# Kernel optimization log

Measured on AMD Instinct MI355X. Metric: run time of the kernel, lower is better.

Reference implementation:

```python
import math
import jax, jax.numpy as jnp
from jax import lax
import numpy as np

C, H, W, N, K = 256, 64, 64, 16, 7

def setup_inputs() -> dict:
    key = jax.random.key(0)
    k0, k1, k2, k3, k4 = jax.random.split(key, 5)
    x = jax.random.normal(k0, (N, C, H, W), dtype=jnp.float32)
    p_2_w = 0.02 * jax.random.normal(k1, (1, C, H, 1), dtype=jnp.float32)
    # nn.Conv2d(c, c, (1,5), groups=1, bias=False) -> weight [c, c, 1, 5]
    fan_in = C * 1 * 5
    bound = 1.0 / math.sqrt(fan_in)
    p_3_w = jax.random.uniform(k2, (C, C, 1, 5), dtype=jnp.float32, minval=-bound, maxval=bound)
    p_4_w = 0.02 * jax.random.normal(k3, (1, C, K, 1, 1), dtype=jnp.float32)
    p_6_w = jax.random.uniform(k4, (K, 1), dtype=jnp.float32, minval=-7.0, maxval=7.0)
    return {"x": x, "p_2_w": p_2_w, "p_3_w": p_3_w, "p_4_w": p_4_w, "p_6_w": p_6_w}

def reference(x, p_2_w, p_3_w, p_4_w, p_6_w):
    n, c, h, w = x.shape
    k = p_4_w.shape[2]  # 7 taps
    pad = (k - 1) // 2
    # F.unfold with kernel (1,7), pad (0,3): stack 7 width-shifted copies -> [n,c,7,h,w]
    xp = jnp.pad(x, ((0, 0), (0, 0), (0, 0), (pad, pad)))
    t_1 = jnp.stack([xp[..., i:i + w] for i in range(k)], axis=2)
    # per-(channel,row) scaling then dense 1x5 conv
    t_2 = p_2_w * x
    t_3 = lax.conv_general_dilated(
        t_2, p_3_w, window_strides=(1, 1), padding=[(0, 0), (2, 2)],
        dimension_numbers=("NCHW", "OIHW", "NCHW"))
    # weighted tap-sum: (p_4_w * t_1) contracted over taps with p_6_w[:,0]
    t_4 = p_4_w * t_1
    t_6 = jnp.einsum("nckhw,kf->ncfhw", t_4, p_6_w)[:, :, 0]  # [n,c,h,w]
    t_5 = jax.nn.relu(x)
    s = h * w
    # channel-attention matrix [n,c,c]
    t_7 = jnp.einsum("ncs,nds->ncd", t_3.reshape(n, c, s), t_6.reshape(n, c, s))
    t_7 = t_7 * (1.0 / math.sqrt(s))
    # bmm(t_5^T, t_7) -> [n,s,d]; permuting to [n,d,h,w] == einsum 'ncs,ncd->nds'
    out = jnp.einsum("ncs,ncd->nds", t_5.reshape(n, c, s), t_7)
    out = out * (1.0 / math.sqrt(c))
    return out.reshape(n, c, h, w)
```

## Files before the change

kernel.cpp:

```cpp
#include <hip/hip_runtime.h>
#include <hip/hip_bf16.h>

typedef __attribute__((ext_vector_type(8))) short bf16x8;
typedef __attribute__((ext_vector_type(4))) float f32x4;

#define NB 16
#define CD 256
#define HD 64
#define WD 64
#define WP 68
#define SD 4096
#define KU 1280

__device__ __forceinline__ void gload16(const void* g, void* lds) {
  __builtin_amdgcn_global_load_lds(
      (const __attribute__((address_space(1))) unsigned int*)g,
      (__attribute__((address_space(3))) unsigned int*)lds, 16, 0, 0);
}

__global__ __launch_bounds__(256) void prep_w3(const float* __restrict__ p3,
                                               __hip_bfloat16* __restrict__ A) {
  int id = blockIdx.x * 256 + threadIdx.x;
  if (id >= CD * KU) return;
  int o = id / KU;
  int r = id - o * KU;
  int j = r >> 8;
  int c = r & 255;
  A[id] = __float2bfloat16(p3[(o * CD + c) * 5 + j]);
}

__global__ __launch_bounds__(256) void prep_x(const float* __restrict__ x,
                                              const float* __restrict__ p2,
                                              const float* __restrict__ p4,
                                              const float* __restrict__ p6,
                                              __hip_bfloat16* __restrict__ t2p,
                                              __hip_bfloat16* __restrict__ t5T,
                                              __hip_bfloat16* __restrict__ t6) {
  int h = blockIdx.x;
  int c0 = blockIdx.y * 64;
  int n = blockIdx.z;
  __shared__ float xl[64][67];
  __shared__ float p2l[64];
  __shared__ float wtl[64][8];
  int t = threadIdx.x;

  if (t < 64) p2l[t] = p2[(c0 + t) * HD + h];
  for (int idx = t; idx < 448; idx += 256) {
    int c = idx / 7, k = idx - c * 7;
    wtl[c][k] = p4[(c0 + c) * 7 + k] * p6[k];
  }

  {
    int cq = t >> 4;
    int w4 = (t & 15) * 4;
#pragma unroll
    for (int cc = 0; cc < 4; ++cc) {
      int cl = cc * 16 + cq;
      const float4 xv = *reinterpret_cast<const float4*>(
          &x[(((size_t)n * CD + c0 + cl) * HD + h) * WD + w4]);
      xl[cl][w4 + 0] = xv.x;
      xl[cl][w4 + 1] = xv.y;
      xl[cl][w4 + 2] = xv.z;
      xl[cl][w4 + 3] = xv.w;
    }
  }
  __syncthreads();

  __hip_bfloat16* t2pn = t2p + (size_t)n * HD * WP * CD;
#pragma unroll
  for (int ii = 0; ii < 2; ++ii) {
    int w = (t >> 3) + ii * 32;
    int cb = (t & 7) * 8;
    __hip_bfloat16 o2[8], o5[8];
#pragma unroll
    for (int j = 0; j < 8; ++j) {
      float xv = xl[cb + j][w];
      o5[j] = __float2bfloat16(fmaxf(xv, 0.f));
      o2[j] = __float2bfloat16(p2l[cb + j] * xv);
    }
    size_t s = (size_t)h * 64 + w;
    *reinterpret_cast<bf16x8*>(&t5T[((size_t)n * SD + s) * CD + c0 + cb]) =
        *reinterpret_cast<const bf16x8*>(o5);
    *reinterpret_cast<bf16x8*>(&t2pn[((size_t)h * WP + w + 2) * CD + c0 + cb]) =
        *reinterpret_cast<const bf16x8*>(o2);
  }
  if (t < 32) {
    int pi = t >> 3;
    int wp = (pi < 2) ? pi : pi + 64;
    int cb = (t & 7) * 8;
    bf16x8 z = (bf16x8){0, 0, 0, 0, 0, 0, 0, 0};
    *reinterpret_cast<bf16x8*>(&t2pn[((size_t)h * WP + wp) * CD + c0 + cb]) = z;
  }

#pragma unroll
  for (int ii = 0; ii < 2; ++ii) {
    int cl = (t >> 3) + ii * 32;
    int w8 = (t & 7) * 8;
    float hx[14];
#pragma unroll
    for (int m = 0; m < 14; ++m) {
      int wi = w8 - 3 + m;
      hx[m] = (wi >= 0 && wi < 64) ? xl[cl][wi] : 0.f;
    }
    float wt[7];
#pragma unroll
    for (int k = 0; k < 7; ++k) wt[k] = wtl[cl][k];
    __hip_bfloat16 o6[8];
#pragma unroll
    for (int u = 0; u < 8; ++u) {
      float acc = 0.f;
#pragma unroll
      for (int k = 0; k < 7; ++k) acc += wt[k] * hx[u + k];
      o6[u] = __float2bfloat16(acc);
    }
    *reinterpret_cast<bf16x8*>(&t6[((size_t)n * CD + c0 + cl) * SD + h * 64 + w8]) =
        *reinterpret_cast<const bf16x8*>(o6);
  }
}

#define STAGE_A(c, kt, d)                                                              \
  gload16(Ab + (size_t)((c) * 64 + wv * 8 + (lane >> 3)) * 2560 + (kt) * 128 + cbsrc,  \
          (char*)lds + (d) * 65536 + (c) * 8192 + wv * 1024)
#define STAGE_B(j, kt, d)                                                              \
  gload16(t2pb + (size_t)(s0 + (j) * 64 + wv * 8 + (lane >> 3) + 4 * (sb * 4 + (j))) * 512 + \
                     (kt) * 128 + cbsrc,                                               \
          (char*)lds + (d) * 65536 + 32768 + (j) * 8192 + wv * 1024)

#define LDAV(d, MH, AV)                                                                \
  do {                                                                                 \
    const __hip_bfloat16* pA =                                                         \
        lds + (d) * 32768 + (wm * 128 + (MH) * 64 + l16) * 64;                         \
    _Pragma("unroll") for (int ks = 0; ks < 2; ++ks) {                                 \
      int cb = (ks * 32 + lg * 8) ^ lxor;                                              \
      _Pragma("unroll") for (int mf = 0; mf < 4; ++mf)                                 \
          AV[ks * 4 + mf] = *reinterpret_cast<const bf16x8*>(pA + mf * 1024 + cb);     \
    }                                                                                  \
  } while (0)

#define LDBV(d, NH, BV)                                                                \
  do {                                                                                 \
    const __hip_bfloat16* pB =                                                         \
        lds + (d) * 32768 + 16384 + (wn * 64 + (NH) * 32 + l16) * 64;                  \
    _Pragma("unroll") for (int ks = 0; ks < 2; ++ks) {                                 \
      int cb = (ks * 32 + lg * 8) ^ lxor;                                              \
      _Pragma("unroll") for (int nf = 0; nf < 2; ++nf)                                 \
          BV[ks * 2 + nf] = *reinterpret_cast<const bf16x8*>(pB + nf * 1024 + cb);     \
    }                                                                                  \
  } while (0)

#define MFMAQ(MH, NH, AV, BV)                                                          \
  do {                                                                                 \
    __builtin_amdgcn_s_setprio(1);                                                     \
    _Pragma("unroll") for (int ks = 0; ks < 2; ++ks)                                   \
        _Pragma("unroll") for (int mf = 0; mf < 4; ++mf)                               \
            _Pragma("unroll") for (int nf = 0; nf < 2; ++nf)                           \
                acc[(MH) * 4 + mf][(NH) * 2 + nf] = __builtin_amdgcn_mfma_f32_16x16x32_bf16( \
                    AV[ks * 4 + mf], BV[ks * 2 + nf], acc[(MH) * 4 + mf][(NH) * 2 + nf], \
                    0, 0, 0);                                                          \
    __builtin_amdgcn_s_setprio(0);                                                     \
  } while (0)

#define VMWAIT(N) asm volatile("s_waitcnt vmcnt(" #N ")" ::: "memory")
#define BARRIER() __builtin_amdgcn_s_barrier()

__global__ __launch_bounds__(512, 2) void gemm_b8(const __hip_bfloat16* __restrict__ A,
                                                  const __hip_bfloat16* __restrict__ t2p,
                                                  __hip_bfloat16* __restrict__ t3) {
  __shared__ __align__(16) __hip_bfloat16 lds[65536];
  const int n = blockIdx.z;
  const int sb = blockIdx.x;
  const int t = threadIdx.x;
  const int wv = t >> 6, lane = t & 63;
  const int wm = wv >> 2, wn = wv & 3;
  const int l16 = lane & 15, lg = lane >> 4;
  const int s0 = sb * 256;
  const char* Ab = (const char*)A;
  const char* t2pb = (const char*)(t2p + (size_t)n * HD * WP * CD);
  const int cbsrc = ((lane & 7) ^ (lane >> 3)) * 16;
  const int lxor = (l16 & 7) * 8;

  f32x4 acc[8][4];
#pragma unroll
  for (int i = 0; i < 8; ++i)
#pragma unroll
    for (int j = 0; j < 4; ++j) acc[i][j] = (f32x4){0.f, 0.f, 0.f, 0.f};

  bf16x8 av0[8], av1[8], bvA[4], bvB[4];

  STAGE_B(0, 0, 0); STAGE_B(1, 0, 0); STAGE_B(2, 0, 0); STAGE_B(3, 0, 0);
  STAGE_A(0, 0, 0); STAGE_A(1, 0, 0); STAGE_A(2, 0, 0); STAGE_A(3, 0, 0);
  VMWAIT(0);
  BARRIER();
  LDAV(0, 0, av0);
  LDBV(0, 0, bvA);

  for (int kt = 0; kt < 19; ++kt) {
    const int cur = kt & 1, nxt = cur ^ 1, kn = kt + 1;
    LDAV(cur, 1, av1);
    LDBV(cur, 1, bvB);
    MFMAQ(0, 0, av0, bvA);
    STAGE_B(0, kn, nxt); STAGE_B(1, kn, nxt); STAGE_B(2, kn, nxt); STAGE_B(3, kn, nxt);
    BARRIER();
    MFMAQ(0, 1, av0, bvB);
    STAGE_A(0, kn, nxt); STAGE_A(1, kn, nxt); STAGE_A(2, kn, nxt); STAGE_A(3, kn, nxt);
    BARRIER();
    MFMAQ(1, 0, av1, bvA);
    BARRIER();
    MFMAQ(1, 1, av1, bvB);
    VMWAIT(0);
    BARRIER();
    LDAV(nxt, 0, av0);
    LDBV(nxt, 0, bvA);
  }
  LDAV(1, 1, av1);
  LDBV(1, 1, bvB);
  MFMAQ(0, 0, av0, bvA);
  MFMAQ(0, 1, av0, bvB);
  MFMAQ(1, 0, av1, bvA);
  MFMAQ(1, 1, av1, bvB);

  __hip_bfloat16* t3n = t3 + (size_t)n * CD * SD;
#pragma unroll
  for (int im = 0; im < 8; ++im)
#pragma unroll
    for (int in = 0; in < 4; ++in) {
      int row0 = wm * 128 + im * 16 + lg * 4;
      int col = s0 + wn * 64 + in * 16 + l16;
#pragma unroll
      for (int r = 0; r < 4; ++r)
        t3n[(size_t)(row0 + r) * SD + col] = __float2bfloat16(acc[im][in][r]);
    }
}

__global__ __launch_bounds__(256) void gemm_c_part(const __hip_bfloat16* __restrict__ t6,
                                                   const __hip_bfloat16* __restrict__ t3,
                                                   float* __restrict__ P4) {
  __shared__ __align__(16) __hip_bfloat16 lA[64 * 64];
  __shared__ __align__(16) __hip_bfloat16 lB[64 * 64];
  int bx = blockIdx.x;
  int cbk = bx & 3, kc = bx >> 2;
  int db = blockIdx.y;
  int n = blockIdx.z;
  int t = threadIdx.x;
  int wave = t >> 6, lane = t & 63;
  int wm = wave >> 1, wn = wave & 1;
  int l16 = lane & 15, lg = lane >> 4;
  int d0 = db * 64;
  int c0 = cbk * 64;
  int kbase = kc * 1024;
  const __hip_bfloat16* An = t6 + (size_t)n * CD * SD + kbase;
  const __hip_bfloat16* Bn = t3 + (size_t)n * CD * SD + kbase;

  int srow = t >> 3;
  int scol = (t & 7) * 8;
  const __hip_bfloat16* gA0 = An + (size_t)(d0 + srow) * SD + scol;
  const __hip_bfloat16* gA1 = An + (size_t)(d0 + srow + 32) * SD + scol;
  const __hip_bfloat16* gB0 = Bn + (size_t)(c0 + srow) * SD + scol;
  const __hip_bfloat16* gB1 = Bn + (size_t)(c0 + srow + 32) * SD + scol;
  __hip_bfloat16* lAd0 = &lA[t * 8];
  __hip_bfloat16* lAd1 = &lA[t * 8 + 32 * 64];
  __hip_bfloat16* lBd0 = &lB[t * 8];
  __hip_bfloat16* lBd1 = &lB[t * 8 + 32 * 64];

  f32x4 acc[2][2];
#pragma unroll
  for (int mi = 0; mi < 2; ++mi)
#pragma unroll
    for (int ni = 0; ni < 2; ++ni) acc[mi][ni] = (f32x4){0.f, 0.f, 0.f, 0.f};

  gload16(gA0, lAd0);
  gload16(gA1, lAd1);
  gload16(gB0, lBd0);
  gload16(gB1, lBd1);

  for (int k = 0; k < 16; ++k) {
    __syncthreads();
#pragma unroll
    for (int ks = 0; ks < 2; ++ks) {
      bf16x8 a[2], b[2];
#pragma unroll
      for (int mi = 0; mi < 2; ++mi)
        a[mi] = *reinterpret_cast<const bf16x8*>(&lA[(wm * 32 + mi * 16 + l16) * 64 + ks * 32 + lg * 8]);
#pragma unroll
      for (int ni = 0; ni < 2; ++ni)
        b[ni] = *reinterpret_cast<const bf16x8*>(&lB[(wn * 32 + ni * 16 + l16) * 64 + ks * 32 + lg * 8]);
#pragma unroll
      for (int mi = 0; mi < 2; ++mi)
#pragma unroll
        for (int ni = 0; ni < 2; ++ni)
          acc[mi][ni] = __builtin_amdgcn_mfma_f32_16x16x32_bf16(a[mi], b[ni], acc[mi][ni], 0, 0, 0);
    }
    __syncthreads();
    if (k < 15) {
      int kk = (k + 1) * 64;
      gload16(gA0 + kk, lAd0);
      gload16(gA1 + kk, lAd1);
      gload16(gB0 + kk, lBd0);
      gload16(gB1 + kk, lBd1);
    }
  }

  float* Pn = P4 + ((size_t)kc * NB + n) * CD * CD;
#pragma unroll
  for (int mi = 0; mi < 2; ++mi)
#pragma unroll
    for (int ni = 0; ni < 2; ++ni) {
      int col = c0 + wn * 32 + ni * 16 + l16;
      int row0 = d0 + wm * 32 + mi * 16 + lg * 4;
#pragma unroll
      for (int r = 0; r < 4; ++r)
        Pn[(size_t)(row0 + r) * CD + col] = acc[mi][ni][r];
    }
}

__global__ __launch_bounds__(256) void reduce_P(const float* __restrict__ P4,
                                                __hip_bfloat16* __restrict__ P) {
  size_t i = ((size_t)blockIdx.x * 256 + threadIdx.x) * 4;
  const size_t stride = (size_t)NB * CD * CD;
  float4 a = *reinterpret_cast<const float4*>(P4 + i);
  float4 b = *reinterpret_cast<const float4*>(P4 + stride + i);
  float4 c = *reinterpret_cast<const float4*>(P4 + 2 * stride + i);
  float4 d = *reinterpret_cast<const float4*>(P4 + 3 * stride + i);
  __hip_bfloat16 o[4];
  o[0] = __float2bfloat16((a.x + b.x + c.x + d.x) * 0.015625f);
  o[1] = __float2bfloat16((a.y + b.y + c.y + d.y) * 0.015625f);
  o[2] = __float2bfloat16((a.z + b.z + c.z + d.z) * 0.015625f);
  o[3] = __float2bfloat16((a.w + b.w + c.w + d.w) * 0.015625f);
  *reinterpret_cast<short4*>(&P[i]) = *reinterpret_cast<const short4*>(o);
}

#define DSTAGE_A(i, kk)                                                                \
  gload16(Pb + (size_t)((i) * 32 + wv4 * 8 + (lane >> 3)) * 512 + (kk) * 128 + cbsrc,  \
          (char*)lA + (i) * 4096 + wv4 * 1024)
#define DSTAGE_B(i, kk)                                                                \
  gload16(Tb + (size_t)(s0 + (i) * 32 + wv4 * 8 + (lane >> 3)) * 512 + (kk) * 128 + cbsrc, \
          (char*)lB + (i) * 4096 + wv4 * 1024)

__global__ __launch_bounds__(256, 2) void gemm_d(const __hip_bfloat16* __restrict__ P,
                                                 const __hip_bfloat16* __restrict__ t5T,
                                                 float* __restrict__ out) {
  __shared__ __align__(16) __hip_bfloat16 lA[256 * 64];
  __shared__ __align__(16) __hip_bfloat16 lB[128 * 64];
  const int n = blockIdx.z;
  const int sb = blockIdx.x;
  const int t = threadIdx.x;
  const int wv4 = t >> 6, lane = t & 63;
  const int wm = wv4 >> 1, wn = wv4 & 1;
  const int l16 = lane & 15, lg = lane >> 4;
  const int s0 = sb * 128;
  const char* Pb = (const char*)(P + (size_t)n * CD * CD);
  const char* Tb = (const char*)(t5T + (size_t)n * SD * CD);
  const int cbsrc = ((lane & 7) ^ (lane >> 3)) * 16;
  const int lxor = (l16 & 7) * 8;

  f32x4 acc[8][4];
#pragma unroll
  for (int i = 0; i < 8; ++i)
#pragma unroll
    for (int j = 0; j < 4; ++j) acc[i][j] = (f32x4){0.f, 0.f, 0.f, 0.f};

#pragma unroll
  for (int i = 0; i < 8; ++i) DSTAGE_A(i, 0);
#pragma unroll
  for (int i = 0; i < 4; ++i) DSTAGE_B(i, 0);

  for (int k = 0; k < 4; ++k) {
    __syncthreads();
#pragma unroll
    for (int ks = 0; ks < 2; ++ks) {
      int cb = (ks * 32 + lg * 8) ^ lxor;
      bf16x8 a[8], b[4];
#pragma unroll
      for (int mf = 0; mf < 8; ++mf)
        a[mf] = *reinterpret_cast<const bf16x8*>(&lA[(wm * 128 + mf * 16 + l16) * 64 + cb]);
#pragma unroll
      for (int nf = 0; nf < 4; ++nf)
        b[nf] = *reinterpret_cast<const bf16x8*>(&lB[(wn * 64 + nf * 16 + l16) * 64 + cb]);
#pragma unroll
      for (int mf = 0; mf < 8; ++mf)
#pragma unroll
        for (int nf = 0; nf < 4; ++nf)
          acc[mf][nf] = __builtin_amdgcn_mfma_f32_16x16x32_bf16(a[mf], b[nf], acc[mf][nf], 0, 0, 0);
    }
    __syncthreads();
    if (k < 3) {
      int kk = k + 1;
#pragma unroll
      for (int i = 0; i < 8; ++i) DSTAGE_A(i, kk);
#pragma unroll
      for (int i = 0; i < 4; ++i) DSTAGE_B(i, kk);
    }
  }

  float* outn = out + (size_t)n * CD * SD;
#pragma unroll
  for (int mf = 0; mf < 8; ++mf)
#pragma unroll
    for (int nf = 0; nf < 4; ++nf) {
      int col = s0 + wn * 64 + nf * 16 + l16;
      int row0 = wm * 128 + mf * 16 + lg * 4;
#pragma unroll
      for (int r = 0; r < 4; ++r)
        outn[(size_t)(row0 + r) * SD + col] = acc[mf][nf][r] * 0.0625f;
    }
}

extern "C" void kernel_launch(void* const* d_in, const int* in_sizes, int n_in,
                              void* d_out, int out_size, void* d_ws, size_t ws_size,
                              hipStream_t stream) {
  const float* x = (const float*)d_in[0];
  const float* p2 = (const float*)d_in[1];
  const float* p3 = (const float*)d_in[2];
  const float* p4 = (const float*)d_in[3];
  const float* p6 = (const float*)d_in[4];

  char* ws = (char*)d_ws;
  size_t off = 0;
  __hip_bfloat16* A = (__hip_bfloat16*)(ws + off);
  off += (size_t)CD * KU * 2;
  size_t t2p_off = off;
  __hip_bfloat16* t2p = (__hip_bfloat16*)(ws + off);
  off += (size_t)NB * HD * WP * CD * 2;
  __hip_bfloat16* t5T = (__hip_bfloat16*)(ws + off);
  off += (size_t)NB * SD * CD * 2;
  __hip_bfloat16* t6 = (__hip_bfloat16*)(ws + off);
  off += (size_t)NB * CD * SD * 2;
  __hip_bfloat16* t3 = (__hip_bfloat16*)(ws + off);
  off += (size_t)NB * CD * SD * 2;
  float* P4 = (float*)(ws + t2p_off);
  __hip_bfloat16* P = (__hip_bfloat16*)(ws + t2p_off + (size_t)4 * NB * CD * CD * 4);

  float* out = (float*)d_out;

  prep_w3<<<dim3((CD * KU + 255) / 256), 256, 0, stream>>>(p3, A);
  prep_x<<<dim3(HD, 4, NB), 256, 0, stream>>>(x, p2, p4, p6, t2p, t5T, t6);
  gemm_b8<<<dim3(16, 1, NB), 512, 0, stream>>>(A, t2p, t3);
  gemm_c_part<<<dim3(16, 4, NB), 256, 0, stream>>>(t6, t3, P4);
  reduce_P<<<dim3((NB * CD * CD / 4) / 256), 256, 0, stream>>>(P4, P);
  gemm_d<<<dim3(32, 1, NB), 256, 0, stream>>>(P, t5T, out);
}
```

Baseline: 133.3 us.

## Fold weight prep into prep_x and restructure conv GEMM into 4-stage K=32 pipeline

The separate prep_w3 launch is removed and the bf16 weight conversion is done by the first blocks of prep_x, saving one kernel launch. The main conv GEMM is rewritten from a double-buffered K=64 schedule with multiple barriers per step into a 4-deep ring of K=32 stages with one barrier per stage, a new XOR swizzle, and loads issued two stages ahead. This aims to overlap global-to-LDS traffic with MFMA work and cut barrier count, at the cost of more loop iterations and a different bank-conflict pattern.

```diff
diff --git a/kernel.cpp b/kernel.cpp
--- a/kernel.cpp
+++ b/kernel.cpp
@@ -18,24 +18,15 @@
       (__attribute__((address_space(3))) unsigned int*)lds, 16, 0, 0);
 }
 
-__global__ __launch_bounds__(256) void prep_w3(const float* __restrict__ p3,
-                                               __hip_bfloat16* __restrict__ A) {
-  int id = blockIdx.x * 256 + threadIdx.x;
-  if (id >= CD * KU) return;
-  int o = id / KU;
-  int r = id - o * KU;
-  int j = r >> 8;
-  int c = r & 255;
-  A[id] = __float2bfloat16(p3[(o * CD + c) * 5 + j]);
-}
-
 __global__ __launch_bounds__(256) void prep_x(const float* __restrict__ x,
                                               const float* __restrict__ p2,
                                               const float* __restrict__ p4,
                                               const float* __restrict__ p6,
+                                              const float* __restrict__ p3,
                                               __hip_bfloat16* __restrict__ t2p,
                                               __hip_bfloat16* __restrict__ t5T,
-                                              __hip_bfloat16* __restrict__ t6) {
+                                              __hip_bfloat16* __restrict__ t6,
+                                              __hip_bfloat16* __restrict__ A) {
   int h = blockIdx.x;
   int c0 = blockIdx.y * 64;
   int n = blockIdx.z;
@@ -43,6 +34,18 @@
   __shared__ float p2l[64];
   __shared__ float wtl[64][8];
   int t = threadIdx.x;
+
+  {
+    int bid = (n * 64 + h) * 4 + blockIdx.y;
+    int id = bid * 256 + t;
+    if (id < CD * KU) {
+      int o = id / KU;
+      int r = id - o * KU;
+      int j = r >> 8;
+      int c = r & 255;
+      A[id] = __float2bfloat16(p3[(o * CD + c) * 5 + j]);
+    }
+  }
 
   if (t < 64) p2l[t] = p2[(c0 + t) * HD + h];
   for (int idx = t; idx < 448; idx += 256) {
@@ -118,55 +121,47 @@
   }
 }
 
-#define STAGE_A(c, kt, d)                                                              \
-  gload16(Ab + (size_t)((c) * 64 + wv * 8 + (lane >> 3)) * 2560 + (kt) * 128 + cbsrc,  \
-          (char*)lds + (d) * 65536 + (c) * 8192 + wv * 1024)
-#define STAGE_B(j, kt, d)                                                              \
-  gload16(t2pb + (size_t)(s0 + (j) * 64 + wv * 8 + (lane >> 3) + 4 * (sb * 4 + (j))) * 512 + \
-                     (kt) * 128 + cbsrc,                                               \
-          (char*)lds + (d) * 65536 + 32768 + (j) * 8192 + wv * 1024)
-
-#define LDAV(d, MH, AV)                                                                \
+#define VMWAIT(N) asm volatile("s_waitcnt vmcnt(" #N ")" ::: "memory")
+#define BARRIER() __builtin_amdgcn_s_barrier()
+
+#define ST4(kt, bi)                                                                    \
   do {                                                                                 \
-    const __hip_bfloat16* pA =                                                         \
-        lds + (d) * 32768 + (wm * 128 + (MH) * 64 + l16) * 64;                         \
-    _Pragma("unroll") for (int ks = 0; ks < 2; ++ks) {                                 \
-      int cb = (ks * 32 + lg * 8) ^ lxor;                                              \
-      _Pragma("unroll") for (int mf = 0; mf < 4; ++mf)                                 \
-          AV[ks * 4 + mf] = *reinterpret_cast<const bf16x8*>(pA + mf * 1024 + cb);     \
+    char* dst = lb + ((bi) << 15) + t * 16;                                            \
+    gload16(gA0 + (kt) * 64, dst);                                                     \
+    gload16(gA1 + (kt) * 64, dst + 8192);                                              \
+    gload16(gB0 + (kt) * 64, dst + 16384);                                             \
+    gload16(gB1 + (kt) * 64, dst + 24576);                                             \
+  } while (0)
+
+#define LDF(bi, AV, BV)                                                                \
+  do {                                                                                 \
+    const char* ba = lb + ((bi) << 15);                                                \
+    _Pragma("unroll") for (int mf = 0; mf < 8; ++mf) {                                 \
+      int row = wm * 128 + mf * 16 + l16;                                              \
+      AV[mf] = *reinterpret_cast<const bf16x8*>(ba + row * 64 + ((lg ^ rxor) * 16));   \
+    }                                                                                  \
+    _Pragma("unroll") for (int nf = 0; nf < 4; ++nf) {                                 \
+      int row = wn * 64 + nf * 16 + l16;                                               \
+      BV[nf] = *reinterpret_cast<const bf16x8*>(ba + 16384 + row * 64 +                \
+                                                ((lg ^ rxor) * 16));                   \
     }                                                                                  \
   } while (0)
 
-#define LDBV(d, NH, BV)                                                                \
-  do {                                                                                 \
-    const __hip_bfloat16* pB =                                                         \
-        lds + (d) * 32768 + 16384 + (wn * 64 + (NH) * 32 + l16) * 64;                  \
-    _Pragma("unroll") for (int ks = 0; ks < 2; ++ks) {                                 \
-      int cb = (ks * 32 + lg * 8) ^ lxor;                                              \
-      _Pragma("unroll") for (int nf = 0; nf < 2; ++nf)                                 \
-          BV[ks * 2 + nf] = *reinterpret_cast<const bf16x8*>(pB + nf * 1024 + cb);     \
-    }                                                                                  \
-  } while (0)
-
-#define MFMAQ(MH, NH, AV, BV)                                                          \
+#define MM(AV, BV)                                                                     \
   do {                                                                                 \
     __builtin_amdgcn_s_setprio(1);                                                     \
-    _Pragma("unroll") for (int ks = 0; ks < 2; ++ks)                                   \
-        _Pragma("unroll") for (int mf = 0; mf < 4; ++mf)                               \
-            _Pragma("unroll") for (int nf = 0; nf < 2; ++nf)                           \
-                acc[(MH) * 4 + mf][(NH) * 2 + nf] = __builtin_amdgcn_mfma_f32_16x16x32_bf16( \
-                    AV[ks * 4 + mf], BV[ks * 2 + nf], acc[(MH) * 4 + mf][(NH) * 2 + nf], \
-                    0, 0, 0);                                                          \
+    _Pragma("unroll") for (int mf = 0; mf < 8; ++mf)                                   \
+        _Pragma("unroll") for (int nf = 0; nf < 4; ++nf)                               \
+            acc[mf][nf] = __builtin_amdgcn_mfma_f32_16x16x32_bf16(AV[mf], BV[nf],      \
+                                                                  acc[mf][nf], 0, 0, 0); \
     __builtin_amdgcn_s_setprio(0);                                                     \
   } while (0)
-
-#define VMWAIT(N) asm volatile("s_waitcnt vmcnt(" #N ")" ::: "memory")
-#define BARRIER() __builtin_amdgcn_s_barrier()
 
 __global__ __launch_bounds__(512, 2) void gemm_b8(const __hip_bfloat16* __restrict__ A,
                                                   const __hip_bfloat16* __restrict__ t2p,
                                                   __hip_bfloat16* __restrict__ t3) {
   __shared__ __align__(16) __hip_bfloat16 lds[65536];
+  char* lb = (char*)lds;
   const int n = blockIdx.z;
   const int sb = blockIdx.x;
   const int t = threadIdx.x;
@@ -174,10 +169,17 @@
   const int wm = wv >> 2, wn = wv & 3;
   const int l16 = lane & 15, lg = lane >> 4;
   const int s0 = sb * 256;
+  const int rxor = (l16 >> 1) & 3;
   const char* Ab = (const char*)A;
   const char* t2pb = (const char*)(t2p + (size_t)n * HD * WP * CD);
-  const int cbsrc = ((lane & 7) ^ (lane >> 3)) * 16;
-  const int lxor = (l16 & 7) * 8;
+  const int cbsrc = ((t & 3) ^ ((t >> 3) & 3)) * 16;
+
+  const int r0 = t >> 2;
+  const char* gA0 = Ab + (size_t)r0 * 2560 + cbsrc;
+  const char* gA1 = Ab + (size_t)(r0 + 128) * 2560 + cbsrc;
+  const int s1 = s0 + r0, s2 = s0 + r0 + 128;
+  const char* gB0 = t2pb + (size_t)(s1 + 4 * (s1 >> 6)) * 512 + cbsrc;
+  const char* gB1 = t2pb + (size_t)(s2 + 4 * (s2 >> 6)) * 512 + cbsrc;
 
   f32x4 acc[8][4];
 #pragma unroll
@@ -185,39 +187,42 @@
 #pragma unroll
     for (int j = 0; j < 4; ++j) acc[i][j] = (f32x4){0.f, 0.f, 0.f, 0.f};
 
-  bf16x8 av0[8], av1[8], bvA[4], bvB[4];
-
-  STAGE_B(0, 0, 0); STAGE_B(1, 0, 0); STAGE_B(2, 0, 0); STAGE_B(3, 0, 0);
-  STAGE_A(0, 0, 0); STAGE_A(1, 0, 0); STAGE_A(2, 0, 0); STAGE_A(3, 0, 0);
+  bf16x8 avX[8], bvX[4], avY[8], bvY[4];
+
+  ST4(0, 0);
+  ST4(1, 1);
+  VMWAIT(4);
+  BARRIER();
+  LDF(0, avX, bvX);
+
+  for (int k2 = 0; k2 < 18; ++k2) {
+    const int kt = k2 * 2;
+    ST4(kt + 2, (kt + 2) & 3);
+    MM(avX, bvX);
+    VMWAIT(4);
+    BARRIER();
+    LDF((kt + 1) & 3, avY, bvY);
+    ST4(kt + 3, (kt + 3) & 3);
+    MM(avY, bvY);
+    VMWAIT(4);
+    BARRIER();
+    LDF((kt + 2) & 3, avX, bvX);
+  }
+  ST4(38, 2);
+  MM(avX, bvX);
+  VMWAIT(4);
+  BARRIER();
+  LDF(1, avY, bvY);
+  ST4(39, 3);
+  MM(avY, bvY);
+  VMWAIT(4);
+  BARRIER();
+  LDF(2, avX, bvX);
+  MM(avX, bvX);
   VMWAIT(0);
   BARRIER();
-  LDAV(0, 0, av0);
-  LDBV(0, 0, bvA);
-
-  for (int kt = 0; kt < 19; ++kt) {
-    const int cur = kt & 1, nxt = cur ^ 1, kn = kt + 1;
-    LDAV(cur, 1, av1);
-    LDBV(cur, 1, bvB);
-    MFMAQ(0, 0, av0, bvA);
-    STAGE_B(0, kn, nxt); STAGE_B(1, kn, nxt); STAGE_B(2, kn, nxt); STAGE_B(3, kn, nxt);
-    BARRIER();
-    MFMAQ(0, 1, av0, bvB);
-    STAGE_A(0, kn, nxt); STAGE_A(1, kn, nxt); STAGE_A(2, kn, nxt); STAGE_A(3, kn, nxt);
-    BARRIER();
-    MFMAQ(1, 0, av1, bvA);
-    BARRIER();
-    MFMAQ(1, 1, av1, bvB);
-    VMWAIT(0);
-    BARRIER();
-    LDAV(nxt, 0, av0);
-    LDBV(nxt, 0, bvA);
-  }
-  LDAV(1, 1, av1);
-  LDBV(1, 1, bvB);
-  MFMAQ(0, 0, av0, bvA);
-  MFMAQ(0, 1, av0, bvB);
-  MFMAQ(1, 0, av1, bvA);
-  MFMAQ(1, 1, av1, bvB);
+  LDF(3, avY, bvY);
+  MM(avY, bvY);
 
   __hip_bfloat16* t3n = t3 + (size_t)n * CD * SD;
 #pragma unroll
@@ -432,8 +437,7 @@
 
   float* out = (float*)d_out;
 
-  prep_w3<<<dim3((CD * KU + 255) / 256), 256, 0, stream>>>(p3, A);
-  prep_x<<<dim3(HD, 4, NB), 256, 0, stream>>>(x, p2, p4, p6, t2p, t5T, t6);
+  prep_x<<<dim3(HD, 4, NB), 256, 0, stream>>>(x, p2, p4, p6, p3, t2p, t5T, t6, A);
   gemm_b8<<<dim3(16, 1, NB), 512, 0, stream>>>(A, t2p, t3);
   gemm_c_part<<<dim3(16, 4, NB), 256, 0, stream>>>(t6, t3, P4);
   reduce_P<<<dim3((NB * CD * CD / 4) / 256), 256, 0, stream>>>(P4, P);
```

New measurement: 128.9 us (median of 2 runs). 1.03x faster.
